# Kernel optimization log

Hardware: AMD Instinct MI355X
Metric: run time of the kernel (lower is better)

Reference implementation:

```python
import jax, jax.numpy as jnp
import numpy as np

B, N, C, OUT, E = 8, 16384, 128, 256, 262144


def setup_inputs() -> dict:
    key = jax.random.key(0)
    k1, k2, k3 = jax.random.split(key, 3)
    x = jax.random.normal(k1, (B, N, C), dtype=jnp.float32)
    edge_index = jax.random.randint(k2, (2, E), 0, N, dtype=jnp.int64)
    W = jax.random.normal(k3, (C, OUT), dtype=jnp.float32) * 0.02
    b = jnp.zeros((OUT,), dtype=jnp.float32)
    return {"x": x, "edge_index": edge_index, "W": W, "b": b}


def reference(x, edge_index, W, b):
    # x: (B, N, C); edge_index: (2, E) shared across the batch (as in the torch code,
    # which repeats row/col B times with batch offsets -> equivalent to per-batch segment max).
    row, col = edge_index[0], edge_index[1]
    n = x.shape[1]

    def agg_one(xb):  # xb: (N, C)
        x_j = xb[col]  # gather neighbor features, (E, C)
        a = jax.ops.segment_max(x_j, row, num_segments=n)  # amax scatter-reduce
        # nodes with no incoming edge: torch fills -1e9 then zeros them; segment_max gives -inf
        return jnp.where(jnp.isfinite(a), a, 0.0)

    aggr = jax.vmap(agg_one)(x) - x  # max-relative: max_j(x_j) - x_i, (B, N, C)
    h = jnp.einsum("bnc,co->bno", aggr, W) + b
    return jax.nn.gelu(h, approximate=False)  # torch nn.GELU() is exact erf GELU
```

## Files before the change

kernel.cpp:

```cpp
#include <hip/hip_runtime.h>
#include <hip/hip_bf16.h>

#define B_   8
#define N_   16384
#define C_   128
#define OUT_ 256
#define E_   262144

#define DEG_OFF  0u
#define OFFS_OFF 16384u
#define SCOL_OFF 32832u
#define WT_OFF   294976u
#define XBF_OFF  311360u
#define AGGR_OFF 8699968u

typedef __attribute__((ext_vector_type(8))) short bf16x8;
typedef __attribute__((ext_vector_type(4))) float f32x4;

__device__ __forceinline__ unsigned short f2bf(float f) {
  unsigned u = __float_as_uint(f);
  u += 0x7FFFu + ((u >> 16) & 1u);
  return (unsigned short)(u >> 16);
}
__device__ __forceinline__ float gelu_exact(float v) {
  return 0.5f * v * (1.0f + erff(v * 0.70710678118654752f));
}

__global__ __launch_bounds__(256) void k_fused1(const float* __restrict__ x,
                                                const unsigned* __restrict__ eidx,
                                                const float* __restrict__ W,
                                                unsigned* __restrict__ ws) {
  const unsigned bid = blockIdx.x, tid = threadIdx.x;
  if (bid < 16384u) {
    unsigned i = bid * 256u + tid;
    float4 v = ((const float4*)x)[i];
    uint2 o;
    o.x = (unsigned)f2bf(v.x) | ((unsigned)f2bf(v.y) << 16);
    o.y = (unsigned)f2bf(v.z) | ((unsigned)f2bf(v.w) << 16);
    ((uint2*)(ws + XBF_OFF))[i] = o;
  } else if (bid < 17408u) {
    __shared__ int flag32;
    if (tid == 0) flag32 = 0;
    __syncthreads();
    unsigned e = (bid - 16384u) * 256u + tid;
    if (eidx[2u * e + 1u] != 0u) flag32 = 1;
    __syncthreads();
    int row = flag32 ? (int)eidx[e] : (int)((const long long*)eidx)[e];
    atomicAdd(ws + DEG_OFF + (unsigned)row, 1u);
  } else {
    unsigned t = (bid - 17408u) * 256u + tid;
    unsigned n = t >> 7, k = t & 127u;
    ((unsigned short*)(ws + WT_OFF))[n * 128u + k] = f2bf(W[k * 256u + n]);
  }
}

__global__ __launch_bounds__(1024) void k_scan(unsigned* __restrict__ ws) {
  __shared__ unsigned part[1024];
  const unsigned t = threadIdx.x;
  unsigned* deg  = ws + DEG_OFF;
  unsigned* offs = ws + OFFS_OFF;
  unsigned v[16], s = 0;
#pragma unroll
  for (int j = 0; j < 16; ++j) { v[j] = deg[t * 16 + j]; s += v[j]; }
  part[t] = s;
  __syncthreads();
  for (int d = 1; d < 1024; d <<= 1) {
    unsigned add = (t >= (unsigned)d) ? part[t - d] : 0u;
    __syncthreads();
    part[t] += add;
    __syncthreads();
  }
  unsigned base = (t == 0u) ? 0u : part[t - 1];
#pragma unroll
  for (int j = 0; j < 16; ++j) {
    unsigned pv = v[j];
    offs[t * 16 + j] = base;
    deg[t * 16 + j] = base;
    base += pv;
  }
  if (t == 1023u) offs[16384] = base;
}

__global__ __launch_bounds__(256) void k_build(const unsigned* __restrict__ eidx,
                                               unsigned* __restrict__ ws) {
  __shared__ int flag32;
  if (threadIdx.x == 0) flag32 = 0;
  __syncthreads();
  unsigned e = blockIdx.x * 256u + threadIdx.x;
  if (eidx[2u * e + 1u] != 0u) flag32 = 1;
  __syncthreads();
  int row, col;
  if (flag32) {
    row = (int)eidx[e];
    col = (int)eidx[e + E_];
  } else {
    const long long* p = (const long long*)eidx;
    row = (int)p[e];
    col = (int)p[e + E_];
  }
  unsigned pos = atomicAdd(ws + DEG_OFF + (unsigned)row, 1u);
  ws[SCOL_OFF + pos] = (unsigned)col;
}

__global__ __launch_bounds__(256) void k_aggr4(const uint4* __restrict__ xbf4,
                                               const unsigned* __restrict__ ws,
                                               uint4* __restrict__ aggr4) {
  const unsigned bi = blockIdx.x;
  const unsigned b  = bi & 7u;
  const unsigned rg = bi >> 3;
  const unsigned row = (rg << 2) | (threadIdx.x >> 6);
  const unsigned lane = threadIdx.x & 63u;
  const unsigned g  = lane >> 4;
  const unsigned ln = lane & 15u;
  const unsigned* offs = ws + OFFS_OFF;
  const unsigned* scol = ws + SCOL_OFF;
  const uint4* xb = xbf4 + ((size_t)b << 18);

  const unsigned j0 = offs[row], e1 = offs[row + 1];
  const bool has = (j0 < e1);
  const unsigned deg = e1 - j0;
  const unsigned d64 = deg < 64u ? deg : 64u;

  unsigned cpre = 0u;
  if (has) {
    unsigned ci = j0 + lane;
    cpre = scol[ci < e1 ? ci : (e1 - 1u)];
  }

  float mlo[4], mhi[4];
#pragma unroll
  for (int r = 0; r < 4; ++r) { mlo[r] = -INFINITY; mhi[r] = -INFINITY; }

#define MAX1(a, r)                                                          \
  mhi[r] = fmaxf(mhi[r], __uint_as_float(a));                               \
  mlo[r] = fmaxf(mlo[r], __uint_as_float((a) << 16));
#define MAX2(a, c, r)                                                       \
  mhi[r] = fmaxf(mhi[r], fmaxf(__uint_as_float(a), __uint_as_float(c)));    \
  mlo[r] = fmaxf(mlo[r],                                                    \
      fmaxf(__uint_as_float((a) << 16), __uint_as_float((c) << 16)));

  unsigned t = 0u;
  while (t + 8u <= d64) {
    unsigned c0 = (unsigned)__shfl((int)cpre, (int)(t + g));
    unsigned c1 = (unsigned)__shfl((int)cpre, (int)(t + 4u + g));
    uint4 u0 = xb[((size_t)c0 << 4) + ln];
    uint4 u1 = xb[((size_t)c1 << 4) + ln];
    MAX2(u0.x, u1.x, 0) MAX2(u0.y, u1.y, 1)
    MAX2(u0.z, u1.z, 2) MAX2(u0.w, u1.w, 3)
    t += 8u;
  }
  if (t + 4u <= d64) {
    unsigned c = (unsigned)__shfl((int)cpre, (int)(t + g));
    uint4 u = xb[((size_t)c << 4) + ln];
    MAX1(u.x, 0) MAX1(u.y, 1) MAX1(u.z, 2) MAX1(u.w, 3)
    t += 4u;
  }
  {
    unsigned rem = d64 - t;
    unsigned c = (unsigned)__shfl((int)cpre, (int)((t + g) & 63u));
    if (g < rem) {
      uint4 u = xb[((size_t)c << 4) + ln];
      MAX1(u.x, 0) MAX1(u.y, 1) MAX1(u.z, 2) MAX1(u.w, 3)
    }
  }
  for (unsigned j = j0 + 64u; j < e1; j += 4u) {
    unsigned r2 = e1 - j;
    if (g < (r2 < 4u ? r2 : 4u)) {
      unsigned c = scol[j + g];
      uint4 u = xb[((size_t)c << 4) + ln];
      MAX1(u.x, 0) MAX1(u.y, 1) MAX1(u.z, 2) MAX1(u.w, 3)
    }
  }
#undef MAX1
#undef MAX2

#pragma unroll
  for (int r = 0; r < 4; ++r) {
    mlo[r] = fmaxf(mlo[r], __shfl_xor(mlo[r], 16, 64));
    mhi[r] = fmaxf(mhi[r], __shfl_xor(mhi[r], 16, 64));
  }
#pragma unroll
  for (int r = 0; r < 4; ++r) {
    mlo[r] = fmaxf(mlo[r], __shfl_xor(mlo[r], 32, 64));
    mhi[r] = fmaxf(mhi[r], __shfl_xor(mhi[r], 32, 64));
  }

  if (g == 0u) {
    const uint4 xw = xb[((size_t)row << 4) + ln];
    unsigned xv[4] = {xw.x, xw.y, xw.z, xw.w};
    unsigned ox[4];
#pragma unroll
    for (int r = 0; r < 4; ++r) {
      float vlo = has ? mlo[r] : 0.0f;
      float vhi = has ? __uint_as_float(__float_as_uint(mhi[r]) & 0xFFFF0000u)
                      : 0.0f;
      unsigned lo = f2bf(vlo - __uint_as_float(xv[r] << 16));
      unsigned hi = f2bf(vhi - __uint_as_float(xv[r] & 0xFFFF0000u));
      ox[r] = lo | (hi << 16);
    }
    uint4 o = {ox[0], ox[1], ox[2], ox[3]};
    aggr4[(((size_t)b << 14) + row) * 16u + ln] = o;
  }
}

__global__ __launch_bounds__(256, 4) void k_gemm(const unsigned short* __restrict__ aggr,
                                                 const unsigned short* __restrict__ Wt,
                                                 const float* __restrict__ bias,
                                                 float* __restrict__ out) {
  __shared__ unsigned short Wt_sm[128 * 136];
  const int tid = threadIdx.x;
  const int nbase = blockIdx.x * 128;
  const int mbase = blockIdx.y * 64;

#pragma unroll
  for (int i = 0; i < 8; ++i) {
    int slot = i * 256 + tid;
    int n = slot >> 4, k8 = slot & 15;
    uint4 u = *(const uint4*)(Wt + (size_t)(nbase + n) * 128 + k8 * 8);
    *(uint4*)&Wt_sm[n * 136 + k8 * 8] = u;
  }
  __syncthreads();

  const int lane = tid & 63;
  const int wv = tid >> 6;
  const int ln = lane & 15;
  const int q = lane >> 4;

  const unsigned short* arow = aggr + (size_t)(mbase + wv * 16 + ln) * 128 + q * 8;
  bf16x8 af[4];
#pragma unroll
  for (int kc = 0; kc < 4; ++kc) af[kc] = *(const bf16x8*)(arow + kc * 32);

  f32x4 acc[8];
#pragma unroll
  for (int f = 0; f < 8; ++f) acc[f] = (f32x4){0.f, 0.f, 0.f, 0.f};

#pragma unroll
  for (int kc = 0; kc < 4; ++kc) {
#pragma unroll
    for (int f = 0; f < 8; ++f) {
      bf16x8 bf = *(const bf16x8*)&Wt_sm[(f * 16 + ln) * 136 + kc * 32 + q * 8];
      acc[f] = __builtin_amdgcn_mfma_f32_16x16x32_bf16(af[kc], bf, acc[f], 0, 0, 0);
    }
  }

#pragma unroll
  for (int f = 0; f < 8; ++f) {
    int n = nbase + f * 16 + ln;
    float bv = bias[n];
#pragma unroll
    for (int r = 0; r < 4; ++r) {
      int m = mbase + wv * 16 + q * 4 + r;
      out[(size_t)m * 256 + n] = gelu_exact(acc[f][r] + bv);
    }
  }
}

extern "C" void kernel_launch(void* const* d_in, const int* in_sizes, int n_in,
                              void* d_out, int out_size, void* d_ws, size_t ws_size,
                              hipStream_t stream) {
  const float* x      = (const float*)d_in[0];
  const unsigned* eid = (const unsigned*)d_in[1];
  const float* W      = (const float*)d_in[2];
  const float* bia    = (const float*)d_in[3];
  float* out          = (float*)d_out;
  unsigned* ws        = (unsigned*)d_ws;

  unsigned short* Wt   = (unsigned short*)(ws + WT_OFF);
  unsigned short* aggr = (unsigned short*)(ws + AGGR_OFF);

  hipMemsetAsync(ws + DEG_OFF, 0, 16384 * sizeof(unsigned), stream);
  hipLaunchKernelGGL(k_fused1, dim3(17536),   dim3(256),  0, stream, x, eid, W, ws);
  hipLaunchKernelGGL(k_scan,   dim3(1),       dim3(1024), 0, stream, ws);
  hipLaunchKernelGGL(k_build,  dim3(1024),    dim3(256),  0, stream, eid, ws);
  hipLaunchKernelGGL(k_aggr4,  dim3(32768),   dim3(256),  0, stream,
                     (const uint4*)(ws + XBF_OFF), ws, (uint4*)(ws + AGGR_OFF));
  hipLaunchKernelGGL(k_gemm,   dim3(2, 2048), dim3(256),  0, stream,
                     aggr, Wt, bia, out);
}
```

Before: 299.7 us.

## Replace CSR build with fixed-width adjacency table plus overflow list

The count/scan/build pipeline for a CSR adjacency is replaced by a single-pass fixed 64-slot-per-row table filled with atomics inside the prep kernel, with an overflow list for rows of degree above 64. This removes the single-block scan kernel and the separate build kernel, saving two launches and their serialization. The aggregation loop is also unrolled to 16 neighbors per iteration for more loads in flight. The trade-off is a larger workspace table and a linear scan of the overflow list for high-degree rows.

Result: faster. 284.5 us (-5.1%).

```diff
diff --git a/kernel.cpp b/kernel.cpp
--- a/kernel.cpp
+++ b/kernel.cpp
@@ -7,12 +7,13 @@
 #define OUT_ 256
 #define E_   262144
 
-#define DEG_OFF  0u
-#define OFFS_OFF 16384u
-#define SCOL_OFF 32832u
-#define WT_OFF   294976u
-#define XBF_OFF  311360u
-#define AGGR_OFF 8699968u
+#define CNT_OFF  0u
+#define OVFC_OFF 16384u
+#define OVF_OFF  16448u
+#define TAB_OFF  540736u
+#define WT_OFF   1589312u
+#define XBF_OFF  1605696u
+#define AGGR_OFF 9994304u
 
 typedef __attribute__((ext_vector_type(8))) short bf16x8;
 typedef __attribute__((ext_vector_type(4))) float f32x4;
@@ -26,10 +27,10 @@
   return 0.5f * v * (1.0f + erff(v * 0.70710678118654752f));
 }
 
-__global__ __launch_bounds__(256) void k_fused1(const float* __restrict__ x,
-                                                const unsigned* __restrict__ eidx,
-                                                const float* __restrict__ W,
-                                                unsigned* __restrict__ ws) {
+__global__ __launch_bounds__(256) void k_prep(const float* __restrict__ x,
+                                              const unsigned* __restrict__ eidx,
+                                              const float* __restrict__ W,
+                                              unsigned* __restrict__ ws) {
   const unsigned bid = blockIdx.x, tid = threadIdx.x;
   if (bid < 16384u) {
     unsigned i = bid * 256u + tid;
@@ -45,8 +46,23 @@
     unsigned e = (bid - 16384u) * 256u + tid;
     if (eidx[2u * e + 1u] != 0u) flag32 = 1;
     __syncthreads();
-    int row = flag32 ? (int)eidx[e] : (int)((const long long*)eidx)[e];
-    atomicAdd(ws + DEG_OFF + (unsigned)row, 1u);
+    int row, col;
+    if (flag32) {
+      row = (int)eidx[e];
+      col = (int)eidx[e + E_];
+    } else {
+      const long long* p = (const long long*)eidx;
+      row = (int)p[e];
+      col = (int)p[e + E_];
+    }
+    unsigned pos = atomicAdd(ws + CNT_OFF + (unsigned)row, 1u);
+    if (pos < 64u) {
+      ws[TAB_OFF + ((unsigned)row << 6) + pos] = (unsigned)col;
+    } else {
+      unsigned o = atomicAdd(ws + OVFC_OFF, 1u);
+      ws[OVF_OFF + 2u * o]      = (unsigned)row;
+      ws[OVF_OFF + 2u * o + 1u] = (unsigned)col;
+    }
   } else {
     unsigned t = (bid - 17408u) * 256u + tid;
     unsigned n = t >> 7, k = t & 127u;
@@ -54,57 +70,9 @@
   }
 }
 
-__global__ __launch_bounds__(1024) void k_scan(unsigned* __restrict__ ws) {
-  __shared__ unsigned part[1024];
-  const unsigned t = threadIdx.x;
-  unsigned* deg  = ws + DEG_OFF;
-  unsigned* offs = ws + OFFS_OFF;
-  unsigned v[16], s = 0;
-#pragma unroll
-  for (int j = 0; j < 16; ++j) { v[j] = deg[t * 16 + j]; s += v[j]; }
-  part[t] = s;
-  __syncthreads();
-  for (int d = 1; d < 1024; d <<= 1) {
-    unsigned add = (t >= (unsigned)d) ? part[t - d] : 0u;
-    __syncthreads();
-    part[t] += add;
-    __syncthreads();
-  }
-  unsigned base = (t == 0u) ? 0u : part[t - 1];
-#pragma unroll
-  for (int j = 0; j < 16; ++j) {
-    unsigned pv = v[j];
-    offs[t * 16 + j] = base;
-    deg[t * 16 + j] = base;
-    base += pv;
-  }
-  if (t == 1023u) offs[16384] = base;
-}
-
-__global__ __launch_bounds__(256) void k_build(const unsigned* __restrict__ eidx,
-                                               unsigned* __restrict__ ws) {
-  __shared__ int flag32;
-  if (threadIdx.x == 0) flag32 = 0;
-  __syncthreads();
-  unsigned e = blockIdx.x * 256u + threadIdx.x;
-  if (eidx[2u * e + 1u] != 0u) flag32 = 1;
-  __syncthreads();
-  int row, col;
-  if (flag32) {
-    row = (int)eidx[e];
-    col = (int)eidx[e + E_];
-  } else {
-    const long long* p = (const long long*)eidx;
-    row = (int)p[e];
-    col = (int)p[e + E_];
-  }
-  unsigned pos = atomicAdd(ws + DEG_OFF + (unsigned)row, 1u);
-  ws[SCOL_OFF + pos] = (unsigned)col;
-}
-
-__global__ __launch_bounds__(256) void k_aggr4(const uint4* __restrict__ xbf4,
-                                               const unsigned* __restrict__ ws,
-                                               uint4* __restrict__ aggr4) {
+__global__ __launch_bounds__(256) void k_aggr(const uint4* __restrict__ xbf4,
+                                              const unsigned* __restrict__ ws,
+                                              uint4* __restrict__ aggr4) {
   const unsigned bi = blockIdx.x;
   const unsigned b  = bi & 7u;
   const unsigned rg = bi >> 3;
@@ -112,20 +80,14 @@
   const unsigned lane = threadIdx.x & 63u;
   const unsigned g  = lane >> 4;
   const unsigned ln = lane & 15u;
-  const unsigned* offs = ws + OFFS_OFF;
-  const unsigned* scol = ws + SCOL_OFF;
+  const unsigned* tab = ws + TAB_OFF;
   const uint4* xb = xbf4 + ((size_t)b << 18);
 
-  const unsigned j0 = offs[row], e1 = offs[row + 1];
-  const bool has = (j0 < e1);
-  const unsigned deg = e1 - j0;
+  const unsigned deg = ws[CNT_OFF + row];
+  const bool has = (deg != 0u);
   const unsigned d64 = deg < 64u ? deg : 64u;
 
-  unsigned cpre = 0u;
-  if (has) {
-    unsigned ci = j0 + lane;
-    cpre = scol[ci < e1 ? ci : (e1 - 1u)];
-  }
+  const unsigned cpre = tab[(row << 6) + lane];
 
   float mlo[4], mhi[4];
 #pragma unroll
@@ -140,7 +102,22 @@
       fmaxf(__uint_as_float((a) << 16), __uint_as_float((c) << 16)));
 
   unsigned t = 0u;
-  while (t + 8u <= d64) {
+  while (t + 16u <= d64) {
+    unsigned c0 = (unsigned)__shfl((int)cpre, (int)(t + g));
+    unsigned c1 = (unsigned)__shfl((int)cpre, (int)(t + 4u + g));
+    unsigned c2 = (unsigned)__shfl((int)cpre, (int)(t + 8u + g));
+    unsigned c3 = (unsigned)__shfl((int)cpre, (int)(t + 12u + g));
+    uint4 u0 = xb[((size_t)c0 << 4) + ln];
+    uint4 u1 = xb[((size_t)c1 << 4) + ln];
+    uint4 u2 = xb[((size_t)c2 << 4) + ln];
+    uint4 u3 = xb[((size_t)c3 << 4) + ln];
+    MAX2(u0.x, u1.x, 0) MAX2(u0.y, u1.y, 1)
+    MAX2(u0.z, u1.z, 2) MAX2(u0.w, u1.w, 3)
+    MAX2(u2.x, u3.x, 0) MAX2(u2.y, u3.y, 1)
+    MAX2(u2.z, u3.z, 2) MAX2(u2.w, u3.w, 3)
+    t += 16u;
+  }
+  if (t + 8u <= d64) {
     unsigned c0 = (unsigned)__shfl((int)cpre, (int)(t + g));
     unsigned c1 = (unsigned)__shfl((int)cpre, (int)(t + 4u + g));
     uint4 u0 = xb[((size_t)c0 << 4) + ln];
@@ -163,12 +140,15 @@
       MAX1(u.x, 0) MAX1(u.y, 1) MAX1(u.z, 2) MAX1(u.w, 3)
     }
   }
-  for (unsigned j = j0 + 64u; j < e1; j += 4u) {
-    unsigned r2 = e1 - j;
-    if (g < (r2 < 4u ? r2 : 4u)) {
-      unsigned c = scol[j + g];
-      uint4 u = xb[((size_t)c << 4) + ln];
-      MAX1(u.x, 0) MAX1(u.y, 1) MAX1(u.z, 2) MAX1(u.w, 3)
+  if (deg > 64u) {
+    unsigned no = ws[OVFC_OFF];
+    for (unsigned i = 0u; i < no; i += 4u) {
+      unsigned k = i + g;
+      if (k < no && ws[OVF_OFF + 2u * k] == row) {
+        unsigned c = ws[OVF_OFF + 2u * k + 1u];
+        uint4 u = xb[((size_t)c << 4) + ln];
+        MAX1(u.x, 0) MAX1(u.y, 1) MAX1(u.z, 2) MAX1(u.w, 3)
+      }
     }
   }
 #undef MAX1
@@ -269,12 +249,10 @@
   unsigned short* Wt   = (unsigned short*)(ws + WT_OFF);
   unsigned short* aggr = (unsigned short*)(ws + AGGR_OFF);
 
-  hipMemsetAsync(ws + DEG_OFF, 0, 16384 * sizeof(unsigned), stream);
-  hipLaunchKernelGGL(k_fused1, dim3(17536),   dim3(256),  0, stream, x, eid, W, ws);
-  hipLaunchKernelGGL(k_scan,   dim3(1),       dim3(1024), 0, stream, ws);
-  hipLaunchKernelGGL(k_build,  dim3(1024),    dim3(256),  0, stream, eid, ws);
-  hipLaunchKernelGGL(k_aggr4,  dim3(32768),   dim3(256),  0, stream,
+  hipMemsetAsync(ws + CNT_OFF, 0, 16448 * sizeof(unsigned), stream);
+  hipLaunchKernelGGL(k_prep, dim3(17536),   dim3(256), 0, stream, x, eid, W, ws);
+  hipLaunchKernelGGL(k_aggr, dim3(32768),   dim3(256), 0, stream,
                      (const uint4*)(ws + XBF_OFF), ws, (uint4*)(ws + AGGR_OFF));
-  hipLaunchKernelGGL(k_gemm,   dim3(2, 2048), dim3(256),  0, stream,
+  hipLaunchKernelGGL(k_gemm, dim3(2, 2048), dim3(256), 0, stream,
                      aggr, Wt, bia, out);
 }
```
